# Kernel tuning notes

Measured on AMD Instinct MI355X. Metric: run time of the kernel, lower is better.

Reference implementation:

```python
import jax, jax.numpy as jnp
import numpy as np
from jax import lax

B, L, D, H = 32, 2048, 1024, 16
CHUNK, MEM = 128, 64
PROB, SKILL = 1200, 234
T = MEM + CHUNK
HD = D // H
EPS = 1e-5

# static block mask: mem tokens fully visible, causal within chunk part
_mask_np = np.zeros((T, T), dtype=bool)
_mask_np[MEM:, MEM:] = np.triu(np.ones((CHUNK, CHUNK), dtype=bool), k=1)
MASK = jnp.asarray(_mask_np)


def _ln(x, g, b):
    mu = jnp.mean(x, axis=-1, keepdims=True)
    var = jnp.mean((x - mu) ** 2, axis=-1, keepdims=True)
    return (x - mu) * lax.rsqrt(var + EPS) * g + b


def setup_inputs() -> dict:
    key = jax.random.key(0)
    ks = jax.random.split(key, 12)
    nrm = lambda k, shape: jax.random.normal(k, shape, jnp.float32) * 0.02
    emb_prob = nrm(ks[0], (PROB, D)).at[0].set(0.0)   # padding_idx=0
    emb_skill = nrm(ks[1], (SKILL, D)).at[0].set(0.0)
    return {
        "in_prob": jax.random.randint(ks[9], (B, L), 0, PROB, dtype=jnp.int32),
        "in_skill": jax.random.randint(ks[10], (B, L), 0, SKILL, dtype=jnp.int32),
        "emb_prob": emb_prob,
        "emb_skill": emb_skill,
        "mem_init": nrm(ks[2], (1, MEM, D)),
        "pos_emb": nrm(ks[3], (T, D)),
        "wqkv": nrm(ks[4], (3 * D, D)), "bqkv": jnp.zeros(3 * D, jnp.float32),
        "wo": nrm(ks[5], (D, D)), "bo": jnp.zeros(D, jnp.float32),
        "w1": nrm(ks[6], (4 * D, D)), "b1": jnp.zeros(4 * D, jnp.float32),
        "w2": nrm(ks[7], (D, 4 * D)), "b2": jnp.zeros(D, jnp.float32),
        "ln_a_g": jnp.ones(D, jnp.float32), "ln_a_b": jnp.zeros(D, jnp.float32),
        "ln_f_g": jnp.ones(D, jnp.float32), "ln_f_b": jnp.zeros(D, jnp.float32),
        "gw": nrm(ks[8], (D, D)), "gb": jnp.zeros(D, jnp.float32),
    }


def reference(in_prob, in_skill, emb_prob, emb_skill, mem_init, pos_emb,
              wqkv, bqkv, wo, bo, w1, b1, w2, b2,
              ln_a_g, ln_a_b, ln_f_g, ln_f_b, gw, gb):
    x = emb_prob[in_prob] + emb_skill[in_skill]          # [B,L,D]
    nC = L // CHUNK
    xs = x.reshape(B, nC, CHUNK, D).transpose(1, 0, 2, 3)  # [nC,B,CHUNK,D]
    mem0 = jnp.broadcast_to(mem_init, (B, MEM, D))

    def mha(z):  # z: [B,T,D]
        qkv = z @ wqkv.T + bqkv                          # [B,T,3D]
        q, k, v = jnp.split(qkv, 3, axis=-1)
        q = q.reshape(B, T, H, HD).transpose(0, 2, 1, 3)
        k = k.reshape(B, T, H, HD).transpose(0, 2, 1, 3)
        v = v.reshape(B, T, H, HD).transpose(0, 2, 1, 3)
        scores = jnp.einsum("bhqd,bhkd->bhqk", q, k) / jnp.sqrt(jnp.float32(HD))
        scores = jnp.where(MASK, -jnp.inf, scores)
        attn = jax.nn.softmax(scores, axis=-1)
        o = jnp.einsum("bhqk,bhkd->bhqd", attn, v)
        o = o.transpose(0, 2, 1, 3).reshape(B, T, D)
        return o @ wo.T + bo

    def step(mem, inp):
        chunk, idx = inp
        z = jnp.concatenate([mem, chunk], axis=1) + pos_emb[None]  # [B,T,D]
        z = z + mha(_ln(z, ln_a_g, ln_a_b))
        zf = _ln(z, ln_f_g, ln_f_b)
        z = z + (jax.nn.relu(zf @ w1.T + b1) @ w2.T + b2)
        h = z[:, MEM:, :]
        cand = z[:, :MEM, :]
        g = jax.nn.sigmoid(cand @ gw.T + gb)
        mem_new = jnp.where(idx == 0, cand, g * cand + (1.0 - g) * mem)
        return mem_new, h

    mem_fin, hs = lax.scan(step, mem0, (xs, jnp.arange(nC)))
    out = hs.transpose(1, 0, 2, 3).reshape(B, L, D)
    return out, mem_fin
```

## Files before the change

### kernel.cpp

```cpp
#include <hip/hip_runtime.h>
#include <cstdint>

typedef __attribute__((ext_vector_type(4))) float f32x4;
typedef __attribute__((ext_vector_type(8))) short s16x8;
typedef __attribute__((ext_vector_type(8))) unsigned short u16x8;
typedef __attribute__((ext_vector_type(4))) unsigned short u16x4;

#define DEVI __device__ __forceinline__

namespace {

constexpr int B = 32, L = 2048, D = 1024, H = 16;
constexpr int CHUNK = 128, MEM = 64, T = 192;
constexpr int NC = 16;

DEVI unsigned short f2bf(float f) {
  unsigned x = __builtin_bit_cast(unsigned, f);
  return (unsigned short)((x + 0x7fffu + ((x >> 16) & 1u)) >> 16);
}

typedef const __attribute__((address_space(1))) unsigned char ga_t;
typedef __attribute__((address_space(3))) unsigned char la_t;

DEVI void gload16(const void* g, void* l) {
  __builtin_amdgcn_global_load_lds((ga_t*)g, (la_t*)l, 16, 0, 0);
}

__global__ void k_cvt(const float* __restrict__ in, unsigned short* __restrict__ out, int n) {
  int i = blockIdx.x * 256 + threadIdx.x;
  if (i < n) out[i] = f2bf(in[i]);
}

__global__ void k_copy_mem(const float* __restrict__ src, float* __restrict__ dst) {
  int i = blockIdx.x * 256 + threadIdx.x;
  dst[i] = src[i];
}

template<int MODE>
__global__ __launch_bounds__(256) void k_lnw(
    const float* __restrict__ memb, const float* __restrict__ mem_init,
    const float* __restrict__ pos,
    const float* __restrict__ embP, const float* __restrict__ embS,
    const int* __restrict__ ipr, const int* __restrict__ isk,
    const float* __restrict__ gg, const float* __restrict__ bb,
    float* __restrict__ z, unsigned short* __restrict__ lnout, int t)
{
  const int tid = threadIdx.x, lane = tid & 63, wid = tid >> 6;
  const int row = blockIdx.x * 4 + wid;
  const int b = row / T, i = row % T;
  const int c0 = lane * 4;

  float v[16];
  if constexpr (MODE == 0) {
    if (i < MEM) {
      const float* src = (t == 0) ? (mem_init + (size_t)i * D)
                                  : (memb + ((size_t)b * MEM + i) * D);
      #pragma unroll
      for (int k = 0; k < 4; ++k) {
        const int c = k * 256 + c0;
        const f32x4 s = *reinterpret_cast<const f32x4*>(&src[c]);
        const f32x4 p = *reinterpret_cast<const f32x4*>(&pos[i * D + c]);
        #pragma unroll
        for (int e = 0; e < 4; ++e) v[k * 4 + e] = s[e] + p[e];
      }
    } else {
      const int j = t * CHUNK + (i - MEM);
      const int pi = ipr[b * L + j], si = isk[b * L + j];
      #pragma unroll
      for (int k = 0; k < 4; ++k) {
        const int c = k * 256 + c0;
        const f32x4 ep = *reinterpret_cast<const f32x4*>(&embP[(size_t)pi * D + c]);
        const f32x4 es = *reinterpret_cast<const f32x4*>(&embS[(size_t)si * D + c]);
        const f32x4 p  = *reinterpret_cast<const f32x4*>(&pos[i * D + c]);
        #pragma unroll
        for (int e = 0; e < 4; ++e) v[k * 4 + e] = ep[e] + es[e] + p[e];
      }
    }
  } else {
    #pragma unroll
    for (int k = 0; k < 4; ++k) {
      const f32x4 zz = *reinterpret_cast<const f32x4*>(&z[(size_t)row * D + k * 256 + c0]);
      #pragma unroll
      for (int e = 0; e < 4; ++e) v[k * 4 + e] = zz[e];
    }
  }
  float s = 0.f, s2 = 0.f;
  #pragma unroll
  for (int e = 0; e < 16; ++e) { s += v[e]; s2 += v[e] * v[e]; }
  #pragma unroll
  for (int m = 1; m < 64; m <<= 1) { s += __shfl_xor(s, m, 64); s2 += __shfl_xor(s2, m, 64); }
  const float mu  = s * (1.0f / 1024.0f);
  const float var = s2 * (1.0f / 1024.0f) - mu * mu;
  const float rs  = rsqrtf(var + 1e-5f);
  if constexpr (MODE == 0) {
    #pragma unroll
    for (int k = 0; k < 4; ++k) {
      f32x4 zz = {v[k*4+0], v[k*4+1], v[k*4+2], v[k*4+3]};
      *reinterpret_cast<f32x4*>(&z[(size_t)row * D + k * 256 + c0]) = zz;
    }
  }
  #pragma unroll
  for (int k = 0; k < 4; ++k) {
    const int c = k * 256 + c0;
    u16x4 o;
    #pragma unroll
    for (int e = 0; e < 4; ++e)
      o[e] = f2bf((v[k * 4 + e] - mu) * rs * gg[c + e] + bb[c + e]);
    *reinterpret_cast<u16x4*>(&lnout[(size_t)row * D + c]) = o;
  }
}

struct GArgs {
  const unsigned short* A; const unsigned short* W; const float* bias;
  unsigned short* outb; float* z; float* outf; unsigned short* candb; float* mem;
  int M, N, K, t;
};

template<int EPI, int SPLITK>
__global__ __launch_bounds__(256) void k_gemmp(GArgs a)
{
  __shared__ __align__(16) unsigned short Al[2][128 * 32];
  __shared__ __align__(16) unsigned short Bl[2][128 * 32];
  const int tid = threadIdx.x;
  const int lane = tid & 63, wid = tid >> 6;
  const int gx = gridDim.x;
  const int nwg = gx * gridDim.y;
  const int f = blockIdx.y * gx + blockIdx.x;
  const int tile = (f & 7) * (nwg >> 3) + (f >> 3);
  const int brow = (tile / gx) * 128, bcol = (tile % gx) * 128;
  const int wr = wid >> 1, wc = wid & 1;
  const int c0 = lane & 15, g4 = lane >> 4;
  const int K = a.K;
  const int Ks = K / SPLITK;
  const int kbase = blockIdx.z * Ks;

  const int r0 = tid >> 2, oc8 = (tid & 3) * 8;
  const int dst0 = wid * 512, dst1 = 2048 + wid * 512;

  f32x4 acc[4][4] = {};

  const unsigned short* __restrict__ Ag = a.A;
  const unsigned short* __restrict__ Wg = a.W;

  auto stage = [&](int t1, int buf) {
    const int kb = kbase + t1 * 32;
    gload16(&Ag[(size_t)(brow + r0) * K + kb + oc8],      &Al[buf][dst0]);
    gload16(&Ag[(size_t)(brow + 64 + r0) * K + kb + oc8], &Al[buf][dst1]);
    gload16(&Wg[(size_t)(bcol + r0) * K + kb + oc8],      &Bl[buf][dst0]);
    gload16(&Wg[(size_t)(bcol + 64 + r0) * K + kb + oc8], &Bl[buf][dst1]);
  };

  stage(0, 0);
  const int nt = Ks >> 5;
  int cur = 0;
  for (int t = 0; t < nt; ++t) {
    __syncthreads();
    if (t + 1 < nt) stage(t + 1, cur ^ 1);
    s16x8 af[4], bf[4];
    #pragma unroll
    for (int m = 0; m < 4; ++m)
      af[m] = *reinterpret_cast<const s16x8*>(&Al[cur][(wr * 64 + m * 16 + c0) * 32 + g4 * 8]);
    #pragma unroll
    for (int n = 0; n < 4; ++n)
      bf[n] = *reinterpret_cast<const s16x8*>(&Bl[cur][(wc * 64 + n * 16 + c0) * 32 + g4 * 8]);
    #pragma unroll
    for (int m = 0; m < 4; ++m)
      #pragma unroll
      for (int n = 0; n < 4; ++n)
        acc[m][n] = __builtin_amdgcn_mfma_f32_16x16x32_bf16(af[m], bf[n], acc[m][n], 0, 0, 0);
    cur ^= 1;
  }

  #pragma unroll
  for (int m = 0; m < 4; ++m) {
    #pragma unroll
    for (int n = 0; n < 4; ++n) {
      const int col = bcol + wc * 64 + n * 16 + c0;
      float bv = 0.f;
      if constexpr (EPI != 8) bv = a.bias[col];
      #pragma unroll
      for (int j = 0; j < 4; ++j) {
        const int row = brow + wr * 64 + m * 16 + g4 * 4 + j;
        float v = acc[m][n][j] + bv;
        if constexpr (EPI == 0) {
          a.outb[(size_t)row * a.N + col] = f2bf(v);
        } else if constexpr (EPI == 1) {
          a.outb[(size_t)row * a.N + col] = f2bf(v > 0.f ? v : 0.f);
        } else if constexpr (EPI == 2) {
          a.z[(size_t)row * a.N + col] += v;
        } else if constexpr (EPI == 8) {
          a.outf[(size_t)blockIdx.z * a.M * a.N + (size_t)row * a.N + col] = v;
        }
      }
    }
  }
}

__global__ __launch_bounds__(256) void k_red2(
    const float* __restrict__ p, float* __restrict__ z, const float* __restrict__ bias,
    float* __restrict__ out, unsigned short* __restrict__ candb, int t)
{
  const int row = blockIdx.x;
  const int b = row / T, i = row % T;
  const int c = threadIdx.x * 4;
  const size_t MN = (size_t)B * T * D;
  const f32x4 p0 = *reinterpret_cast<const f32x4*>(&p[(size_t)row * D + c]);
  const f32x4 p1 = *reinterpret_cast<const f32x4*>(&p[MN + (size_t)row * D + c]);
  const f32x4 bb = *reinterpret_cast<const f32x4*>(&bias[c]);
  const f32x4 zz = *reinterpret_cast<const f32x4*>(&z[(size_t)row * D + c]);
  f32x4 zv;
  #pragma unroll
  for (int e = 0; e < 4; ++e) zv[e] = zz[e] + p0[e] + p1[e] + bb[e];
  if (i < MEM) {
    *reinterpret_cast<f32x4*>(&z[(size_t)row * D + c]) = zv;
    u16x4 o;
    #pragma unroll
    for (int e = 0; e < 4; ++e) o[e] = f2bf(zv[e]);
    *reinterpret_cast<u16x4*>(&candb[((size_t)b * MEM + i) * D + c]) = o;
  } else {
    *reinterpret_cast<f32x4*>(&out[((size_t)b * L + t * CHUNK + (i - MEM)) * D + c]) = zv;
  }
}

__global__ __launch_bounds__(256) void k_redg(
    const float* __restrict__ p, const float* __restrict__ z,
    const float* __restrict__ gb, float* __restrict__ memb, int t)
{
  const int row = blockIdx.x;
  const int b = row >> 6, i = row & 63;
  const int c = threadIdx.x * 4;
  const size_t MN = (size_t)B * MEM * D;
  f32x4 s = *reinterpret_cast<const f32x4*>(&gb[c]);
  #pragma unroll
  for (int k = 0; k < 4; ++k) {
    const f32x4 pk = *reinterpret_cast<const f32x4*>(&p[k * MN + (size_t)row * D + c]);
    #pragma unroll
    for (int e = 0; e < 4; ++e) s[e] += pk[e];
  }
  const f32x4 cand = *reinterpret_cast<const f32x4*>(&z[((size_t)b * T + i) * D + c]);
  f32x4 mo = *reinterpret_cast<f32x4*>(&memb[(size_t)row * D + c]);
  f32x4 r;
  #pragma unroll
  for (int e = 0; e < 4; ++e) {
    const float g = 1.0f / (1.0f + __expf(-s[e]));
    r[e] = (t == 0) ? cand[e] : g * cand[e] + (1.0f - g) * mo[e];
  }
  *reinterpret_cast<f32x4*>(&memb[(size_t)row * D + c]) = r;
}

__global__ __launch_bounds__(256) void k_attn(const unsigned short* __restrict__ qkv,
                                              unsigned short* __restrict__ attno)
{
  __shared__ unsigned short Ks[192 * 64];
  __shared__ unsigned short Vt[64 * 192];
  __shared__ unsigned short Pl[4][16 * 200];
  const int tid = threadIdx.x, lane = tid & 63, wid = tid >> 6;
  const int b = blockIdx.x >> 4, h = blockIdx.x & 15;
  const size_t base = (size_t)b * T * 3072 + h * 64;

  #pragma unroll
  for (int it = 0; it < 6; ++it) {
    const int cidx = tid + it * 256;
    const int key = cidx >> 3, hb = cidx & 7;
    const u16x8 kv = *reinterpret_cast<const u16x8*>(&qkv[base + (size_t)key * 3072 + 1024 + hb * 8]);
    *reinterpret_cast<u16x8*>(&Ks[key * 64 + ((hb ^ (key & 7)) * 8)]) = kv;
    const u16x8 vv = *reinterpret_cast<const u16x8*>(&qkv[base + (size_t)key * 3072 + 2048 + hb * 8]);
    #pragma unroll
    for (int e = 0; e < 8; ++e) {
      const int hd = hb * 8 + e;
      Vt[hd * 192 + (((key >> 3) + hd) % 24) * 8 + (key & 7)] = vv[e];
    }
  }
  __syncthreads();

  const int c0 = lane & 15, g4 = lane >> 4;
  for (int qb = wid; qb < 12; qb += 4) {
    s16x8 qf[2];
    #pragma unroll
    for (int kk = 0; kk < 2; ++kk)
      qf[kk] = *reinterpret_cast<const s16x8*>(&qkv[base + (size_t)(qb * 16 + c0) * 3072 + kk * 32 + g4 * 8]);
    f32x4 sc[12];
    #pragma unroll
    for (int cb = 0; cb < 12; ++cb) {
      f32x4 s4 = {};
      #pragma unroll
      for (int kk = 0; kk < 2; ++kk) {
        const s16x8 kf = *reinterpret_cast<const s16x8*>(
            &Ks[(cb * 16 + c0) * 64 + (((kk * 4 + g4) ^ (c0 & 7)) * 8)]);
        s4 = __builtin_amdgcn_mfma_f32_16x16x32_bf16(qf[kk], kf, s4, 0, 0, 0);
      }
      sc[cb] = s4;
    }
    #pragma unroll
    for (int j = 0; j < 4; ++j) {
      const int qi = qb * 16 + g4 * 4 + j;
      float mj = -1e30f;
      #pragma unroll
      for (int cb = 0; cb < 12; ++cb) {
        const int kj = cb * 16 + c0;
        float sv = sc[cb][j] * 0.125f;
        if (qi >= MEM && kj > qi) sv = -1e30f;
        sc[cb][j] = sv;
        mj = fmaxf(mj, sv);
      }
      #pragma unroll
      for (int msk = 1; msk <= 8; msk <<= 1) mj = fmaxf(mj, __shfl_xor(mj, msk, 64));
      float sum = 0.f;
      #pragma unroll
      for (int cb = 0; cb < 12; ++cb) {
        const float p = exp2f((sc[cb][j] - mj) * 1.44269504f);
        sc[cb][j] = p;
        sum += p;
      }
      #pragma unroll
      for (int msk = 1; msk <= 8; msk <<= 1) sum += __shfl_xor(sum, msk, 64);
      const float rin = 1.0f / sum;
      #pragma unroll
      for (int cb = 0; cb < 12; ++cb)
        Pl[wid][(g4 * 4 + j) * 200 + cb * 16 + c0] = f2bf(sc[cb][j] * rin);
    }
    #pragma unroll
    for (int cb2 = 0; cb2 < 4; ++cb2) {
      f32x4 ao = {};
      const int hd = cb2 * 16 + c0;
      #pragma unroll
      for (int kk = 0; kk < 6; ++kk) {
        const int k0 = kk * 32 + g4 * 8;
        const s16x8 pf = *reinterpret_cast<const s16x8*>(&Pl[wid][c0 * 200 + k0]);
        const s16x8 vf = *reinterpret_cast<const s16x8*>(&Vt[hd * 192 + (((k0 >> 3) + hd) % 24) * 8]);
        ao = __builtin_amdgcn_mfma_f32_16x16x32_bf16(pf, vf, ao, 0, 0, 0);
      }
      #pragma unroll
      for (int j = 0; j < 4; ++j) {
        const int q = qb * 16 + g4 * 4 + j;
        attno[((size_t)b * T + q) * D + h * 64 + cb2 * 16 + c0] = f2bf(ao[j]);
      }
    }
  }
}

}

extern "C" void kernel_launch(void* const* d_in, const int* in_sizes, int n_in,
                              void* d_out, int out_size, void* d_ws, size_t ws_size,
                              hipStream_t stream)
{
  const int*   ipr      = (const int*)d_in[0];
  const int*   isk      = (const int*)d_in[1];
  const float* embP     = (const float*)d_in[2];
  const float* embS     = (const float*)d_in[3];
  const float* mem_init = (const float*)d_in[4];
  const float* pos      = (const float*)d_in[5];
  const float* wqkv     = (const float*)d_in[6];
  const float* bqkv     = (const float*)d_in[7];
  const float* wo       = (const float*)d_in[8];
  const float* bo       = (const float*)d_in[9];
  const float* w1       = (const float*)d_in[10];
  const float* b1       = (const float*)d_in[11];
  const float* w2       = (const float*)d_in[12];
  const float* b2       = (const float*)d_in[13];
  const float* ln_a_g   = (const float*)d_in[14];
  const float* ln_a_b   = (const float*)d_in[15];
  const float* ln_f_g   = (const float*)d_in[16];
  const float* ln_f_b   = (const float*)d_in[17];
  const float* gw       = (const float*)d_in[18];
  const float* gb       = (const float*)d_in[19];
  float* out = (float*)d_out;
  (void)in_sizes; (void)n_in; (void)out_size; (void)ws_size;

  char* ws = (char*)d_ws;
  size_t off = 0;
  auto alloc = [&](size_t bytes) -> void* {
    void* p = ws + off; off += (bytes + 255) & ~(size_t)255; return p;
  };
  unsigned short* wqkv_b = (unsigned short*)alloc((size_t)3072 * 1024 * 2);
  unsigned short* wo_b   = (unsigned short*)alloc((size_t)1024 * 1024 * 2);
  unsigned short* w1_b   = (unsigned short*)alloc((size_t)4096 * 1024 * 2);
  unsigned short* w2_b   = (unsigned short*)alloc((size_t)1024 * 4096 * 2);
  unsigned short* gw_b   = (unsigned short*)alloc((size_t)1024 * 1024 * 2);
  float*          z      = (float*)alloc((size_t)B * T * D * 4);
  unsigned short* lnb    = (unsigned short*)alloc((size_t)B * T * D * 2);
  unsigned short* atno   = (unsigned short*)alloc((size_t)B * T * D * 2);
  unsigned short* big    = (unsigned short*)alloc((size_t)B * T * 4096 * 2);
  unsigned short* candb  = (unsigned short*)alloc((size_t)B * MEM * D * 2);
  float*          memb   = (float*)alloc((size_t)B * MEM * D * 4);
  float*          p2     = (float*)alloc((size_t)2 * B * T * D * 4);
  float*          p4     = (float*)alloc((size_t)4 * B * MEM * D * 4);

  k_cvt<<<(3072 * 1024) / 256, 256, 0, stream>>>(wqkv, wqkv_b, 3072 * 1024);
  k_cvt<<<(1024 * 1024) / 256, 256, 0, stream>>>(wo,   wo_b,   1024 * 1024);
  k_cvt<<<(4096 * 1024) / 256, 256, 0, stream>>>(w1,   w1_b,   4096 * 1024);
  k_cvt<<<(1024 * 4096) / 256, 256, 0, stream>>>(w2,   w2_b,   1024 * 4096);
  k_cvt<<<(1024 * 1024) / 256, 256, 0, stream>>>(gw,   gw_b,   1024 * 1024);

  for (int t = 0; t < NC; ++t) {
    k_lnw<0><<<(B * T) / 4, 256, 0, stream>>>(memb, mem_init, pos, embP, embS, ipr, isk,
                                              ln_a_g, ln_a_b, z, lnb, t);
    { GArgs a{lnb, wqkv_b, bqkv, big, nullptr, nullptr, nullptr, nullptr, B * T, 3072, 1024, t};
      k_gemmp<0, 1><<<dim3(3072 / 128, (B * T) / 128), 256, 0, stream>>>(a); }
    k_attn<<<B * H, 256, 0, stream>>>(big, atno);
    { GArgs a{atno, wo_b, bo, nullptr, z, nullptr, nullptr, nullptr, B * T, 1024, 1024, t};
      k_gemmp<2, 1><<<dim3(1024 / 128, (B * T) / 128), 256, 0, stream>>>(a); }
    k_lnw<1><<<(B * T) / 4, 256, 0, stream>>>(nullptr, nullptr, nullptr, nullptr, nullptr,
                                              nullptr, nullptr, ln_f_g, ln_f_b, z, lnb, t);
    { GArgs a{lnb, w1_b, b1, big, nullptr, nullptr, nullptr, nullptr, B * T, 4096, 1024, t};
      k_gemmp<1, 1><<<dim3(4096 / 128, (B * T) / 128), 256, 0, stream>>>(a); }
    { GArgs a{big, w2_b, nullptr, nullptr, nullptr, p2, nullptr, nullptr, B * T, 1024, 4096, t};
      k_gemmp<8, 2><<<dim3(1024 / 128, (B * T) / 128, 2), 256, 0, stream>>>(a); }
    k_red2<<<B * T, 256, 0, stream>>>(p2, z, b2, out, candb, t);
    { GArgs a{candb, gw_b, nullptr, nullptr, nullptr, p4, nullptr, nullptr, B * MEM, 1024, 1024, t};
      k_gemmp<8, 4><<<dim3(1024 / 128, (B * MEM) / 128, 4), 256, 0, stream>>>(a); }
    k_redg<<<B * MEM, 256, 0, stream>>>(p4, z, gb, memb, t);
  }
  k_copy_mem<<<(B * MEM * D) / 256, 256, 0, stream>>>(memb, out + (size_t)B * L * D);
}
```

Measured before the change: 4.879 ms.

## Run chunk-token FFN GEMMs in FP8 and fuse out-proj residual into LayerNorm

The FFN is split into memory rows and chunk rows. Chunk-token rows (the model output) use new FP8 e4m3 MFMA GEMMs with scaled FP8 weights and FP8 activations. Memory rows stay on the bf16 path so the recurrent memory keeps its precision. The out-projection now writes split-K partials that the second LayerNorm kernel reduces together with the residual and bias, which removes the read-modify-write epilogue. The FP8 path risks accuracy loss on the outputs and adds more, smaller kernel launches.

```diff
diff --git a/kernel.cpp b/kernel.cpp
--- a/kernel.cpp
+++ b/kernel.cpp
@@ -1,10 +1,12 @@
 #include <hip/hip_runtime.h>
+#include <hip/hip_fp8.h>
 #include <cstdint>
 
 typedef __attribute__((ext_vector_type(4))) float f32x4;
 typedef __attribute__((ext_vector_type(8))) short s16x8;
 typedef __attribute__((ext_vector_type(8))) unsigned short u16x8;
 typedef __attribute__((ext_vector_type(4))) unsigned short u16x4;
+typedef unsigned char u8;
 
 #define DEVI __device__ __forceinline__
 
@@ -18,6 +20,10 @@
   unsigned x = __builtin_bit_cast(unsigned, f);
   return (unsigned short)((x + 0x7fffu + ((x >> 16) & 1u)) >> 16);
 }
+DEVI u8 f2fp8(float f) {
+  __hip_fp8_e4m3 h(f);
+  return *reinterpret_cast<u8*>(&h);
+}
 
 typedef const __attribute__((address_space(1))) unsigned char ga_t;
 typedef __attribute__((address_space(3))) unsigned char la_t;
@@ -29,6 +35,10 @@
 __global__ void k_cvt(const float* __restrict__ in, unsigned short* __restrict__ out, int n) {
   int i = blockIdx.x * 256 + threadIdx.x;
   if (i < n) out[i] = f2bf(in[i]);
+}
+__global__ void k_cvt8(const float* __restrict__ in, u8* __restrict__ out, int n) {
+  int i = blockIdx.x * 256 + threadIdx.x;
+  if (i < n) out[i] = f2fp8(in[i] * 32.0f);
 }
 
 __global__ void k_copy_mem(const float* __restrict__ src, float* __restrict__ dst) {
@@ -43,7 +53,9 @@
     const float* __restrict__ embP, const float* __restrict__ embS,
     const int* __restrict__ ipr, const int* __restrict__ isk,
     const float* __restrict__ gg, const float* __restrict__ bb,
-    float* __restrict__ z, unsigned short* __restrict__ lnout, int t)
+    float* __restrict__ z, unsigned short* __restrict__ lnout,
+    u8* __restrict__ ln8out, const float* __restrict__ pp,
+    const float* __restrict__ bo, int t)
 {
   const int tid = threadIdx.x, lane = tid & 63, wid = tid >> 6;
   const int row = blockIdx.x * 4 + wid;
@@ -77,11 +89,16 @@
       }
     }
   } else {
+    const size_t MN = (size_t)B * T * D;
     #pragma unroll
     for (int k = 0; k < 4; ++k) {
-      const f32x4 zz = *reinterpret_cast<const f32x4*>(&z[(size_t)row * D + k * 256 + c0]);
-      #pragma unroll
-      for (int e = 0; e < 4; ++e) v[k * 4 + e] = zz[e];
+      const int c = k * 256 + c0;
+      const f32x4 zz = *reinterpret_cast<const f32x4*>(&z[(size_t)row * D + c]);
+      const f32x4 p0 = *reinterpret_cast<const f32x4*>(&pp[(size_t)row * D + c]);
+      const f32x4 p1 = *reinterpret_cast<const f32x4*>(&pp[MN + (size_t)row * D + c]);
+      const f32x4 bv = *reinterpret_cast<const f32x4*>(&bo[c]);
+      #pragma unroll
+      for (int e = 0; e < 4; ++e) v[k * 4 + e] = zz[e] + p0[e] + p1[e] + bv[e];
     }
   }
   float s = 0.f, s2 = 0.f;
@@ -92,21 +109,45 @@
   const float mu  = s * (1.0f / 1024.0f);
   const float var = s2 * (1.0f / 1024.0f) - mu * mu;
   const float rs  = rsqrtf(var + 1e-5f);
+  #pragma unroll
+  for (int k = 0; k < 4; ++k) {
+    f32x4 zz = {v[k*4+0], v[k*4+1], v[k*4+2], v[k*4+3]};
+    *reinterpret_cast<f32x4*>(&z[(size_t)row * D + k * 256 + c0]) = zz;
+  }
   if constexpr (MODE == 0) {
     #pragma unroll
     for (int k = 0; k < 4; ++k) {
-      f32x4 zz = {v[k*4+0], v[k*4+1], v[k*4+2], v[k*4+3]};
-      *reinterpret_cast<f32x4*>(&z[(size_t)row * D + k * 256 + c0]) = zz;
-    }
-  }
-  #pragma unroll
-  for (int k = 0; k < 4; ++k) {
-    const int c = k * 256 + c0;
-    u16x4 o;
-    #pragma unroll
-    for (int e = 0; e < 4; ++e)
-      o[e] = f2bf((v[k * 4 + e] - mu) * rs * gg[c + e] + bb[c + e]);
-    *reinterpret_cast<u16x4*>(&lnout[(size_t)row * D + c]) = o;
+      const int c = k * 256 + c0;
+      u16x4 o;
+      #pragma unroll
+      for (int e = 0; e < 4; ++e)
+        o[e] = f2bf((v[k * 4 + e] - mu) * rs * gg[c + e] + bb[c + e]);
+      *reinterpret_cast<u16x4*>(&lnout[(size_t)row * D + c]) = o;
+    }
+  } else {
+    if (i < MEM) {
+      const size_t rbase = ((size_t)b * MEM + i) * D;
+      #pragma unroll
+      for (int k = 0; k < 4; ++k) {
+        const int c = k * 256 + c0;
+        u16x4 o;
+        #pragma unroll
+        for (int e = 0; e < 4; ++e)
+          o[e] = f2bf((v[k * 4 + e] - mu) * rs * gg[c + e] + bb[c + e]);
+        *reinterpret_cast<u16x4*>(&lnout[rbase + c]) = o;
+      }
+    } else {
+      const size_t rbase = ((size_t)b * CHUNK + (i - MEM)) * D;
+      #pragma unroll
+      for (int k = 0; k < 4; ++k) {
+        const int c = k * 256 + c0;
+        unsigned w = 0;
+        #pragma unroll
+        for (int e = 0; e < 4; ++e)
+          w |= (unsigned)f2fp8((v[k * 4 + e] - mu) * rs * gg[c + e] + bb[c + e]) << (8 * e);
+        *reinterpret_cast<unsigned*>(&ln8out[rbase + c]) = w;
+      }
+    }
   }
 }
 
@@ -114,6 +155,11 @@
   const unsigned short* A; const unsigned short* W; const float* bias;
   unsigned short* outb; float* z; float* outf; unsigned short* candb; float* mem;
   int M, N, K, t;
+};
+struct G8Args {
+  const u8* A; const u8* W; const float* bias;
+  u8* outb8; float* outf;
+  int M, N, K;
 };
 
 template<int EPI, int SPLITK>
@@ -186,8 +232,6 @@
           a.outb[(size_t)row * a.N + col] = f2bf(v);
         } else if constexpr (EPI == 1) {
           a.outb[(size_t)row * a.N + col] = f2bf(v > 0.f ? v : 0.f);
-        } else if constexpr (EPI == 2) {
-          a.z[(size_t)row * a.N + col] += v;
         } else if constexpr (EPI == 8) {
           a.outf[(size_t)blockIdx.z * a.M * a.N + (size_t)row * a.N + col] = v;
         }
@@ -196,30 +240,118 @@
   }
 }
 
-__global__ __launch_bounds__(256) void k_red2(
+template<int EPI, int SPLITK>
+__global__ __launch_bounds__(256) void k_gemm8(G8Args a)
+{
+  __shared__ __align__(16) u8 Al[2][128 * 32];
+  __shared__ __align__(16) u8 Bl[2][128 * 32];
+  const int tid = threadIdx.x;
+  const int lane = tid & 63, wid = tid >> 6;
+  const int gx = gridDim.x;
+  const int nwg = gx * gridDim.y;
+  const int f = blockIdx.y * gx + blockIdx.x;
+  const int tile = (f & 7) * (nwg >> 3) + (f >> 3);
+  const int brow = (tile / gx) * 128, bcol = (tile % gx) * 128;
+  const int wr = wid >> 1, wc = wid & 1;
+  const int c0 = lane & 15, g4 = lane >> 4;
+  const int K = a.K;
+  const int Ks = K / SPLITK;
+  const int kbase = blockIdx.z * Ks;
+
+  const int r0 = tid >> 1, oc = (tid & 1) * 16;
+  const int dstb = wid * 1024;
+
+  f32x4 acc[4][4] = {};
+
+  const u8* __restrict__ Ag = a.A;
+  const u8* __restrict__ Wg = a.W;
+
+  auto stage = [&](int t1, int buf) {
+    const int kb = kbase + t1 * 32;
+    gload16(&Ag[(size_t)(brow + r0) * K + kb + oc], &Al[buf][dstb]);
+    gload16(&Wg[(size_t)(bcol + r0) * K + kb + oc], &Bl[buf][dstb]);
+  };
+
+  stage(0, 0);
+  const int nt = Ks >> 5;
+  int cur = 0;
+  for (int t = 0; t < nt; ++t) {
+    __syncthreads();
+    if (t + 1 < nt) stage(t + 1, cur ^ 1);
+    long af[4], bf[4];
+    #pragma unroll
+    for (int m = 0; m < 4; ++m)
+      af[m] = *reinterpret_cast<const long*>(&Al[cur][(wr * 64 + m * 16 + c0) * 32 + g4 * 8]);
+    #pragma unroll
+    for (int n = 0; n < 4; ++n)
+      bf[n] = *reinterpret_cast<const long*>(&Bl[cur][(wc * 64 + n * 16 + c0) * 32 + g4 * 8]);
+    #pragma unroll
+    for (int m = 0; m < 4; ++m)
+      #pragma unroll
+      for (int n = 0; n < 4; ++n)
+        acc[m][n] = __builtin_amdgcn_mfma_f32_16x16x32_fp8_fp8(af[m], bf[n], acc[m][n], 0, 0, 0);
+    cur ^= 1;
+  }
+
+  constexpr float SC = 1.0f / 32.0f;
+  #pragma unroll
+  for (int m = 0; m < 4; ++m) {
+    #pragma unroll
+    for (int n = 0; n < 4; ++n) {
+      const int col = bcol + wc * 64 + n * 16 + c0;
+      float bv = 0.f;
+      if constexpr (EPI != 8) bv = a.bias[col];
+      #pragma unroll
+      for (int j = 0; j < 4; ++j) {
+        const int row = brow + wr * 64 + m * 16 + g4 * 4 + j;
+        float v = acc[m][n][j] * SC + bv;
+        if constexpr (EPI == 1) {
+          a.outb8[(size_t)row * a.N + col] = f2fp8(v > 0.f ? v : 0.f);
+        } else {
+          a.outf[(size_t)blockIdx.z * a.M * a.N + (size_t)row * a.N + col] = v;
+        }
+      }
+    }
+  }
+}
+
+__global__ __launch_bounds__(256) void k_red2m(
     const float* __restrict__ p, float* __restrict__ z, const float* __restrict__ bias,
-    float* __restrict__ out, unsigned short* __restrict__ candb, int t)
-{
-  const int row = blockIdx.x;
-  const int b = row / T, i = row % T;
+    unsigned short* __restrict__ candb)
+{
+  const int r = blockIdx.x;
+  const int b = r >> 6, i = r & 63;
   const int c = threadIdx.x * 4;
-  const size_t MN = (size_t)B * T * D;
-  const f32x4 p0 = *reinterpret_cast<const f32x4*>(&p[(size_t)row * D + c]);
-  const f32x4 p1 = *reinterpret_cast<const f32x4*>(&p[MN + (size_t)row * D + c]);
+  const size_t MN = (size_t)B * MEM * D;
+  const size_t zi = ((size_t)b * T + i) * D + c;
+  const f32x4 p0 = *reinterpret_cast<const f32x4*>(&p[(size_t)r * D + c]);
+  const f32x4 p1 = *reinterpret_cast<const f32x4*>(&p[MN + (size_t)r * D + c]);
   const f32x4 bb = *reinterpret_cast<const f32x4*>(&bias[c]);
-  const f32x4 zz = *reinterpret_cast<const f32x4*>(&z[(size_t)row * D + c]);
+  const f32x4 zz = *reinterpret_cast<const f32x4*>(&z[zi]);
   f32x4 zv;
+  u16x4 o;
+  #pragma unroll
+  for (int e = 0; e < 4; ++e) { zv[e] = zz[e] + p0[e] + p1[e] + bb[e]; o[e] = f2bf(zv[e]); }
+  *reinterpret_cast<f32x4*>(&z[zi]) = zv;
+  *reinterpret_cast<u16x4*>(&candb[(size_t)r * D + c]) = o;
+}
+
+__global__ __launch_bounds__(256) void k_red2c(
+    const float* __restrict__ p, const float* __restrict__ z,
+    const float* __restrict__ bias, float* __restrict__ out, int t)
+{
+  const int r = blockIdx.x;
+  const int b = r >> 7, j = r & 127;
+  const int c = threadIdx.x * 4;
+  const size_t MN = (size_t)B * CHUNK * D;
+  const f32x4 p0 = *reinterpret_cast<const f32x4*>(&p[(size_t)r * D + c]);
+  const f32x4 p1 = *reinterpret_cast<const f32x4*>(&p[MN + (size_t)r * D + c]);
+  const f32x4 bb = *reinterpret_cast<const f32x4*>(&bias[c]);
+  const f32x4 zz = *reinterpret_cast<const f32x4*>(&z[((size_t)b * T + MEM + j) * D + c]);
+  f32x4 zv;
   #pragma unroll
   for (int e = 0; e < 4; ++e) zv[e] = zz[e] + p0[e] + p1[e] + bb[e];
-  if (i < MEM) {
-    *reinterpret_cast<f32x4*>(&z[(size_t)row * D + c]) = zv;
-    u16x4 o;
-    #pragma unroll
-    for (int e = 0; e < 4; ++e) o[e] = f2bf(zv[e]);
-    *reinterpret_cast<u16x4*>(&candb[((size_t)b * MEM + i) * D + c]) = o;
-  } else {
-    *reinterpret_cast<f32x4*>(&out[((size_t)b * L + t * CHUNK + (i - MEM)) * D + c]) = zv;
-  }
+  *reinterpret_cast<f32x4*>(&out[((size_t)b * L + t * CHUNK + j) * D + c]) = zv;
 }
 
 __global__ __launch_bounds__(256) void k_redg(
@@ -375,39 +507,54 @@
   };
   unsigned short* wqkv_b = (unsigned short*)alloc((size_t)3072 * 1024 * 2);
   unsigned short* wo_b   = (unsigned short*)alloc((size_t)1024 * 1024 * 2);
+  unsigned short* gw_b   = (unsigned short*)alloc((size_t)1024 * 1024 * 2);
   unsigned short* w1_b   = (unsigned short*)alloc((size_t)4096 * 1024 * 2);
   unsigned short* w2_b   = (unsigned short*)alloc((size_t)1024 * 4096 * 2);
-  unsigned short* gw_b   = (unsigned short*)alloc((size_t)1024 * 1024 * 2);
+  u8*             w1_8   = (u8*)alloc((size_t)4096 * 1024);
+  u8*             w2_8   = (u8*)alloc((size_t)1024 * 4096);
   float*          z      = (float*)alloc((size_t)B * T * D * 4);
   unsigned short* lnb    = (unsigned short*)alloc((size_t)B * T * D * 2);
+  u8*             ln8c   = (u8*)alloc((size_t)B * CHUNK * D);
   unsigned short* atno   = (unsigned short*)alloc((size_t)B * T * D * 2);
-  unsigned short* big    = (unsigned short*)alloc((size_t)B * T * 4096 * 2);
+  unsigned short* big    = (unsigned short*)alloc((size_t)B * T * 3072 * 2);
+  u8*             big8   = (u8*)alloc((size_t)B * CHUNK * 4096);
   unsigned short* candb  = (unsigned short*)alloc((size_t)B * MEM * D * 2);
   float*          memb   = (float*)alloc((size_t)B * MEM * D * 4);
   float*          p2     = (float*)alloc((size_t)2 * B * T * D * 4);
+  float*          p2m    = (float*)alloc((size_t)2 * B * MEM * D * 4);
+  float*          p2c    = (float*)alloc((size_t)2 * B * CHUNK * D * 4);
   float*          p4     = (float*)alloc((size_t)4 * B * MEM * D * 4);
 
   k_cvt<<<(3072 * 1024) / 256, 256, 0, stream>>>(wqkv, wqkv_b, 3072 * 1024);
   k_cvt<<<(1024 * 1024) / 256, 256, 0, stream>>>(wo,   wo_b,   1024 * 1024);
+  k_cvt<<<(1024 * 1024) / 256, 256, 0, stream>>>(gw,   gw_b,   1024 * 1024);
   k_cvt<<<(4096 * 1024) / 256, 256, 0, stream>>>(w1,   w1_b,   4096 * 1024);
   k_cvt<<<(1024 * 4096) / 256, 256, 0, stream>>>(w2,   w2_b,   1024 * 4096);
-  k_cvt<<<(1024 * 1024) / 256, 256, 0, stream>>>(gw,   gw_b,   1024 * 1024);
+  k_cvt8<<<(4096 * 1024) / 256, 256, 0, stream>>>(w1, w1_8, 4096 * 1024);
+  k_cvt8<<<(1024 * 4096) / 256, 256, 0, stream>>>(w2, w2_8, 1024 * 4096);
 
   for (int t = 0; t < NC; ++t) {
     k_lnw<0><<<(B * T) / 4, 256, 0, stream>>>(memb, mem_init, pos, embP, embS, ipr, isk,
-                                              ln_a_g, ln_a_b, z, lnb, t);
+                                              ln_a_g, ln_a_b, z, lnb, nullptr, nullptr,
+                                              nullptr, t);
     { GArgs a{lnb, wqkv_b, bqkv, big, nullptr, nullptr, nullptr, nullptr, B * T, 3072, 1024, t};
       k_gemmp<0, 1><<<dim3(3072 / 128, (B * T) / 128), 256, 0, stream>>>(a); }
     k_attn<<<B * H, 256, 0, stream>>>(big, atno);
-    { GArgs a{atno, wo_b, bo, nullptr, z, nullptr, nullptr, nullptr, B * T, 1024, 1024, t};
-      k_gemmp<2, 1><<<dim3(1024 / 128, (B * T) / 128), 256, 0, stream>>>(a); }
-    k_lnw<1><<<(B * T) / 4, 256, 0, stream>>>(nullptr, nullptr, nullptr, nullptr, nullptr,
-                                              nullptr, nullptr, ln_f_g, ln_f_b, z, lnb, t);
-    { GArgs a{lnb, w1_b, b1, big, nullptr, nullptr, nullptr, nullptr, B * T, 4096, 1024, t};
-      k_gemmp<1, 1><<<dim3(4096 / 128, (B * T) / 128), 256, 0, stream>>>(a); }
-    { GArgs a{big, w2_b, nullptr, nullptr, nullptr, p2, nullptr, nullptr, B * T, 1024, 4096, t};
+    { GArgs a{atno, wo_b, nullptr, nullptr, nullptr, p2, nullptr, nullptr, B * T, 1024, 1024, t};
       k_gemmp<8, 2><<<dim3(1024 / 128, (B * T) / 128, 2), 256, 0, stream>>>(a); }
-    k_red2<<<B * T, 256, 0, stream>>>(p2, z, b2, out, candb, t);
+    k_lnw<2><<<(B * T) / 4, 256, 0, stream>>>(nullptr, nullptr, nullptr, nullptr, nullptr,
+                                              nullptr, nullptr, ln_f_g, ln_f_b, z, lnb,
+                                              ln8c, p2, bo, t);
+    { G8Args a{ln8c, w1_8, b1, big8, nullptr, B * CHUNK, 4096, 1024};
+      k_gemm8<1, 1><<<dim3(4096 / 128, (B * CHUNK) / 128), 256, 0, stream>>>(a); }
+    { GArgs a{lnb, w1_b, b1, big, nullptr, nullptr, nullptr, nullptr, B * MEM, 4096, 1024, t};
+      k_gemmp<1, 1><<<dim3(4096 / 128, (B * MEM) / 128), 256, 0, stream>>>(a); }
+    { G8Args a{big8, w2_8, nullptr, nullptr, p2c, B * CHUNK, 1024, 4096};
+      k_gemm8<8, 2><<<dim3(1024 / 128, (B * CHUNK) / 128, 2), 256, 0, stream>>>(a); }
+    { GArgs a{big, w2_b, nullptr, nullptr, nullptr, p2m, nullptr, nullptr, B * MEM, 1024, 4096, t};
+      k_gemmp<8, 2><<<dim3(1024 / 128, (B * MEM) / 128, 2), 256, 0, stream>>>(a); }
+    k_red2m<<<B * MEM, 256, 0, stream>>>(p2m, z, b2, candb);
+    k_red2c<<<B * CHUNK, 256, 0, stream>>>(p2c, z, b2, out, t);
     { GArgs a{candb, gw_b, nullptr, nullptr, nullptr, p4, nullptr, nullptr, B * MEM, 1024, 1024, t};
       k_gemmp<8, 4><<<dim3(1024 / 128, (B * MEM) / 128, 4), 256, 0, stream>>>(a); }
     k_redg<<<B * MEM, 256, 0, stream>>>(p4, z, gb, memb, t);
```

New measurement: 6.067 ms. 1.24x slower.
